# Kernel tuning notes

Hardware: AMD Instinct MI355X
Metric: run time of the kernel (lower is better)

## Reference

```python
import jax, jax.numpy as jnp
import numpy as np

V, D, H, L, F, B, S = 512, 512, 8, 6, 2048, 8, 1024
DK = D // H
EPS = 1e-5


def _positional_encoding(max_len, d_model):
    pos = np.arange(max_len, dtype=np.float32)[:, None]
    div = np.exp(np.arange(0, d_model, 2, dtype=np.float32) * (-np.log(10000.0) / d_model))
    pe = np.zeros((max_len, d_model), dtype=np.float32)
    pe[:, 0::2] = np.sin(pos * div)
    pe[:, 1::2] = np.cos(pos * div)
    return jnp.asarray(pe)


def setup_inputs() -> dict:
    key = jax.random.key(0)
    ks = jax.random.split(key, 24)
    xavier = lambda k, shp: jax.random.normal(k, shp, jnp.float32) * np.sqrt(2.0 / (shp[-2] + shp[-1]))
    inp = {
        "input_ids": jax.random.randint(ks[0], (B, S), 0, V),
        "emb": jax.random.normal(ks[1], (V, D), jnp.float32) * 0.02,
        "pe": _positional_encoding(1024, D),
        "Wq": xavier(ks[2], (L, D, D)), "bq": jnp.zeros((L, D)),
        "Wk": xavier(ks[3], (L, D, D)), "bk": jnp.zeros((L, D)),
        "Wv": xavier(ks[4], (L, D, D)), "bv": jnp.zeros((L, D)),
        "Wo": xavier(ks[5], (L, D, D)), "bo": jnp.zeros((L, D)),
        "ln1_g": jnp.ones((L, D)), "ln1_b": jnp.zeros((L, D)),
        "W1": xavier(ks[6], (L, D, F)), "b1": jnp.zeros((L, F)),
        "W2": xavier(ks[7], (L, F, D)), "b2": jnp.zeros((L, D)),
        "ln2_g": jnp.ones((L, D)), "ln2_b": jnp.zeros((L, D)),
        "Wout": xavier(ks[8], (D, V)), "bout": jnp.zeros((V,)),
    }
    return inp


def _ln(x, g, b):
    mu = jnp.mean(x, -1, keepdims=True)
    var = jnp.mean(jnp.square(x - mu), -1, keepdims=True)
    return (x - mu) * jax.lax.rsqrt(var + EPS) * g + b


def reference(input_ids, emb, pe, Wq, bq, Wk, bk, Wv, bv, Wo, bo,
              ln1_g, ln1_b, W1, b1, W2, b2, ln2_g, ln2_b, Wout, bout):
    h = emb[input_ids] * np.sqrt(D) + pe[:S]  # [B,S,D]
    # Faithful to the original mask bug: masked_fill(mask==0, -1e9) fills the
    # LOWER triangle (incl diagonal); raw scores are kept strictly where j > i.
    r = jnp.arange(S)
    keep = r[None, :] > r[:, None]  # [S,S]

    def block(h, p):
        (wq, bq_, wk, bk_, wv, bv_, wo, bo_,
         g1, be1, w1, b1_, w2, b2_, g2, be2) = p
        split = lambda t: t.reshape(B, S, H, DK).transpose(0, 2, 1, 3)
        q = split(h @ wq + bq_)
        k = split(h @ wk + bk_)
        v = split(h @ wv + bv_)
        scores = jnp.einsum('bhqd,bhkd->bhqk', q, k) / np.sqrt(DK)
        scores = jnp.where(keep, scores, -1e9)
        a = jax.nn.softmax(scores, axis=-1)
        o = jnp.einsum('bhqk,bhkd->bhqd', a, v).transpose(0, 2, 1, 3).reshape(B, S, D)
        h = _ln(h + (o @ wo + bo_), g1, be1)
        f = jax.nn.relu(h @ w1 + b1_) @ w2 + b2_
        h = _ln(h + f, g2, be2)
        return h, None

    params = (Wq, bq, Wk, bk, Wv, bv, Wo, bo, ln1_g, ln1_b, W1, b1, W2, b2, ln2_g, ln2_b)
    h, _ = jax.lax.scan(block, h, params)
    return h @ Wout + bout  # logits [B,S,V]
```

## Files before the change

### kernel.cpp

```cpp
#include <hip/hip_runtime.h>

typedef unsigned short u16;
typedef __attribute__((ext_vector_type(8))) short bf16x8;
typedef __attribute__((ext_vector_type(4))) float f32x4;
typedef __attribute__((ext_vector_type(4))) unsigned int uint4v;
typedef __attribute__((ext_vector_type(4))) unsigned short us4;

#define NLAYER 6
#define D_MODEL 512
#define NHEAD 8
#define DKH 64
#define SEQ 1024
#define BATCH 8
#define FFN 2048
#define MROWS (BATCH * SEQ)
#define QKV_LD 1536
#define SCALE_LOG2E 0.18033688011112042f

__device__ __forceinline__ float b2f(u16 u) {
  union { unsigned u32; float f; } x; x.u32 = ((unsigned)u) << 16; return x.f;
}
__device__ __forceinline__ u16 f2b(float f) {
  union { float f; unsigned u; } x; x.f = f;
  unsigned r = x.u + 0x7FFFu + ((x.u >> 16) & 1u);
  return (u16)(r >> 16);
}
__device__ __forceinline__ void gld16(const u16* g, u16* l) {
  __builtin_amdgcn_global_load_lds(
      (const __attribute__((address_space(1))) unsigned int*)g,
      (__attribute__((address_space(3))) unsigned int*)l, 16, 0, 0);
}
__device__ __forceinline__ void barrier_raw() {
  asm volatile("" ::: "memory");
  __builtin_amdgcn_s_barrier();
  asm volatile("" ::: "memory");
}

__global__ __launch_bounds__(256) void transpose_cvt_kernel(
    const float* __restrict__ src, u16* __restrict__ dst, int K, int N, size_t dstZ,
    float scale)
{
  __shared__ float t[32][33];
  const int z = blockIdx.z;
  src += (size_t)z * K * N;
  dst += (size_t)z * dstZ;
  const int n0 = blockIdx.x * 32, k0 = blockIdx.y * 32;
  const int tx = threadIdx.x, ty = threadIdx.y;
#pragma unroll
  for (int i = 0; i < 32; i += 8)
    t[ty + i][tx] = src[(size_t)(k0 + ty + i) * N + n0 + tx];
  __syncthreads();
#pragma unroll
  for (int i = 0; i < 32; i += 8)
    dst[(size_t)(n0 + ty + i) * K + k0 + tx] = f2b(t[tx][ty + i] * scale);
}

__global__ __launch_bounds__(256) void concat_bias_kernel(
    const float* __restrict__ bq, const float* __restrict__ bk,
    const float* __restrict__ bv, float* __restrict__ dst)
{
  const int l = blockIdx.x, t = threadIdx.x;
#pragma unroll
  for (int j = t; j < 512; j += 256) {
    dst[l * QKV_LD + j]        = bq[l * 512 + j] * SCALE_LOG2E;
    dst[l * QKV_LD + 512 + j]  = bk[l * 512 + j];
    dst[l * QKV_LD + 1024 + j] = bv[l * 512 + j];
  }
}

__global__ __launch_bounds__(256) void embed_kernel(
    const int* __restrict__ ids, const float* __restrict__ emb,
    const float* __restrict__ pe, float* __restrict__ Hf, u16* __restrict__ Hb)
{
  const int row = blockIdx.x;
  const int s = row & (SEQ - 1);
  const int id = ids[row];
  const int tid = threadIdx.x;
#pragma unroll
  for (int u = 0; u < 2; ++u) {
    const int d = tid + u * 256;
    float v = emb[(size_t)id * D_MODEL + d] * 22.62741699796952f + pe[(size_t)s * D_MODEL + d];
    Hf[(size_t)row * D_MODEL + d] = v;
    Hb[(size_t)row * D_MODEL + d] = f2b(v);
  }
}

template<int BMT, bool RELU, bool OUTF, bool OUTB, bool VT>
__global__ __launch_bounds__(256) void gemm_kernel(
    const u16* __restrict__ A, const u16* __restrict__ Bt,
    const float* __restrict__ bias,
    float* __restrict__ Cf, u16* __restrict__ Cb, u16* __restrict__ Vtp,
    int M, int N, int K)
{
  constexpr int IT = BMT / 32;
  constexpr int AHALF = BMT * 64;
  constexpr int BHALF = 128 * 64;
  __shared__ __align__(16) u16 As[2 * AHALF];
  __shared__ __align__(16) u16 Bs[2 * BHALF];
  const int tid = threadIdx.x;
  const int bm = blockIdx.x * BMT, bn = blockIdx.y * 128;
  const int wave = tid >> 6, lane = tid & 63;
  const int lm = lane & 15, quad = lane >> 4;
  const int wm = (wave & 1) * (BMT / 2), wn = (wave >> 1) * 64;

  const int sr = tid >> 3;
  const int sc = (tid & 7) ^ (sr & 7);
  const u16* Ap = A  + (size_t)(bm + sr) * K + sc * 8;
  const u16* Bp = Bt + (size_t)(bn + sr) * K + sc * 8;
  u16* lA = As + wave * 512;
  u16* lB = Bs + wave * 512;

  f32x4 acc[IT][4] = {};

  const int nt = K >> 6;
  auto stage = [&](int buf, int t) {
    const size_t ko = (size_t)t << 6;
#pragma unroll
    for (int p = 0; p < BMT / 32; ++p)
      gld16(Ap + (size_t)(p * 32) * K + ko, lA + buf * AHALF + p * 2048);
#pragma unroll
    for (int p = 0; p < 4; ++p)
      gld16(Bp + (size_t)(p * 32) * K + ko, lB + buf * BHALF + p * 2048);
  };

  stage(0, 0);
  __syncthreads();

  for (int t = 0; t < nt; ++t) {
    const int cur = t & 1;
    if (t + 1 < nt) stage(cur ^ 1, t + 1);
    const u16* as = As + cur * AHALF;
    const u16* bs = Bs + cur * BHALF;
#pragma unroll
    for (int kh = 0; kh < 2; ++kh) {
      bf16x8 af[IT], bg[4];
#pragma unroll
      for (int i = 0; i < IT; ++i) {
        const int row = wm + i * 16 + lm;
        af[i] = *(const bf16x8*)&as[row * 64 + (((kh * 4 + quad) ^ (row & 7)) << 3)];
      }
#pragma unroll
      for (int j = 0; j < 4; ++j) {
        const int row = wn + j * 16 + lm;
        bg[j] = *(const bf16x8*)&bs[row * 64 + (((kh * 4 + quad) ^ (row & 7)) << 3)];
      }
#pragma unroll
      for (int i = 0; i < IT; ++i)
#pragma unroll
        for (int j = 0; j < 4; ++j)
          acc[i][j] = __builtin_amdgcn_mfma_f32_16x16x32_bf16(af[i], bg[j], acc[i][j], 0, 0, 0);
    }
    __syncthreads();
  }

  const int mbase = bm + wm + quad * 4;
  const int nbase = bn + wn + lm;
#pragma unroll
  for (int i = 0; i < IT; ++i) {
#pragma unroll
    for (int j = 0; j < 4; ++j) {
      const int n = nbase + j * 16;
      const float bv = bias[n];
      float vv[4];
#pragma unroll
      for (int r = 0; r < 4; ++r) {
        float v = acc[i][j][r] + bv;
        if (RELU) v = fmaxf(v, 0.f);
        vv[r] = v;
      }
      if (VT && n >= 1024) {
        const int hh = (n - 1024) >> 6, d = (n - 1024) & 63;
        const int mm = mbase + i * 16;
        const int bb = mm >> 10, ss = mm & 1023;
        us4 pk;
#pragma unroll
        for (int r = 0; r < 4; ++r) pk[r] = f2b(vv[r]);
        *(us4*)&Vtp[(((size_t)(bb * NHEAD + hh)) * 64 + d) * SEQ + ss] = pk;
      } else {
#pragma unroll
        for (int r = 0; r < 4; ++r) {
          const int m = mbase + i * 16 + r;
          if (OUTF) Cf[(size_t)m * N + n] = vv[r];
          if (OUTB) Cb[(size_t)m * N + n] = f2b(vv[r]);
        }
      }
    }
  }
}

template<bool RELU, bool VT>
__global__ __launch_bounds__(512, 2) void gemm256_kernel(
    const u16* __restrict__ A, const u16* __restrict__ Bt,
    const float* __restrict__ bias,
    u16* __restrict__ Cb, u16* __restrict__ Vtp,
    int M, int N, int K)
{
  extern __shared__ __align__(16) u16 smem[];
  u16* Asm = smem;
  u16* Bsm = smem + 32768;
  const int tid = threadIdx.x;
  const int wave = tid >> 6, lane = tid & 63;
  const int lm = lane & 15, quad = lane >> 4, l7 = lm & 7;
  const int wm = wave >> 2, wn = wave & 3;
  const int bm = blockIdx.x * 256, bn = blockIdx.y * 256;

  const int srow = tid >> 3;
  const int scg = (tid & 7) ^ (srow & 7);
  const u16* Ap = A  + (size_t)(bm + srow) * K + scg * 8;
  const u16* Bp = Bt + (size_t)(bn + srow) * K + scg * 8;
  u16* uA = Asm + wave * 512;
  u16* uB = Bsm + wave * 512;

  f32x4 acc[8][4] = {};

  const int NT = K >> 6;
  auto stage = [&](int buf, int t) {
    const size_t ko = (size_t)t << 6;
#pragma unroll
    for (int p = 0; p < 4; ++p)
      gld16(Ap + (size_t)(p * 64) * K + ko, uA + buf * 16384 + p * 4096);
#pragma unroll
    for (int p = 0; p < 4; ++p)
      gld16(Bp + (size_t)(p * 64) * K + ko, uB + buf * 16384 + p * 4096);
  };

  stage(0, 0);
  __syncthreads();

  const int sl0 = (quad ^ l7) << 3;
  const int sl1 = ((quad + 4) ^ l7) << 3;

#pragma unroll 1
  for (int t = 0; t < NT; ++t) {
    const int cur = t & 1;
    if (t + 1 < NT) stage(cur ^ 1, t + 1);
    const u16* as_ = Asm + cur * 16384 + (wm * 128 + lm) * 64;
    const u16* bs_ = Bsm + cur * 16384 + (wn * 64 + lm) * 64;
    bf16x8 af[4][2], b01[2][2], b23[2][2];
#pragma unroll
    for (int i = 0; i < 4; ++i) {
      af[i][0] = *(const bf16x8*)&as_[i * 1024 + sl0];
      af[i][1] = *(const bf16x8*)&as_[i * 1024 + sl1];
    }
#pragma unroll
    for (int j = 0; j < 2; ++j) {
      b01[j][0] = *(const bf16x8*)&bs_[j * 1024 + sl0];
      b01[j][1] = *(const bf16x8*)&bs_[j * 1024 + sl1];
    }
    __builtin_amdgcn_s_setprio(1);
#pragma unroll
    for (int i = 0; i < 4; ++i)
#pragma unroll
      for (int j = 0; j < 2; ++j) {
        acc[i][j] = __builtin_amdgcn_mfma_f32_16x16x32_bf16(af[i][0], b01[j][0], acc[i][j], 0, 0, 0);
        acc[i][j] = __builtin_amdgcn_mfma_f32_16x16x32_bf16(af[i][1], b01[j][1], acc[i][j], 0, 0, 0);
      }
    __builtin_amdgcn_s_setprio(0);
    barrier_raw();
#pragma unroll
    for (int j = 0; j < 2; ++j) {
      b23[j][0] = *(const bf16x8*)&bs_[(j + 2) * 1024 + sl0];
      b23[j][1] = *(const bf16x8*)&bs_[(j + 2) * 1024 + sl1];
    }
    __builtin_amdgcn_s_setprio(1);
#pragma unroll
    for (int i = 0; i < 4; ++i)
#pragma unroll
      for (int j = 0; j < 2; ++j) {
        acc[i][j + 2] = __builtin_amdgcn_mfma_f32_16x16x32_bf16(af[i][0], b23[j][0], acc[i][j + 2], 0, 0, 0);
        acc[i][j + 2] = __builtin_amdgcn_mfma_f32_16x16x32_bf16(af[i][1], b23[j][1], acc[i][j + 2], 0, 0, 0);
      }
    __builtin_amdgcn_s_setprio(0);
    barrier_raw();
#pragma unroll
    for (int i = 0; i < 4; ++i) {
      af[i][0] = *(const bf16x8*)&as_[(i + 4) * 1024 + sl0];
      af[i][1] = *(const bf16x8*)&as_[(i + 4) * 1024 + sl1];
    }
    __builtin_amdgcn_s_setprio(1);
#pragma unroll
    for (int i = 0; i < 4; ++i)
#pragma unroll
      for (int j = 0; j < 2; ++j) {
        acc[i + 4][j + 2] = __builtin_amdgcn_mfma_f32_16x16x32_bf16(af[i][0], b23[j][0], acc[i + 4][j + 2], 0, 0, 0);
        acc[i + 4][j + 2] = __builtin_amdgcn_mfma_f32_16x16x32_bf16(af[i][1], b23[j][1], acc[i + 4][j + 2], 0, 0, 0);
      }
    __builtin_amdgcn_s_setprio(0);
    barrier_raw();
#pragma unroll
    for (int j = 0; j < 2; ++j) {
      b01[j][0] = *(const bf16x8*)&bs_[j * 1024 + sl0];
      b01[j][1] = *(const bf16x8*)&bs_[j * 1024 + sl1];
    }
    __builtin_amdgcn_s_setprio(1);
#pragma unroll
    for (int i = 0; i < 4; ++i)
#pragma unroll
      for (int j = 0; j < 2; ++j) {
        acc[i + 4][j] = __builtin_amdgcn_mfma_f32_16x16x32_bf16(af[i][0], b01[j][0], acc[i + 4][j], 0, 0, 0);
        acc[i + 4][j] = __builtin_amdgcn_mfma_f32_16x16x32_bf16(af[i][1], b01[j][1], acc[i + 4][j], 0, 0, 0);
      }
    __builtin_amdgcn_s_setprio(0);
    if (t + 1 < NT) {
      asm volatile("s_waitcnt vmcnt(0)" ::: "memory");
      barrier_raw();
    }
  }

  const int mbase = bm + wm * 128 + quad * 4;
  const int nbase = bn + wn * 64 + lm;
#pragma unroll
  for (int i = 0; i < 8; ++i) {
#pragma unroll
    for (int j = 0; j < 4; ++j) {
      const int n = nbase + j * 16;
      const float bv = bias[n];
      float vv[4];
#pragma unroll
      for (int r = 0; r < 4; ++r) {
        float v = acc[i][j][r] + bv;
        if (RELU) v = fmaxf(v, 0.f);
        vv[r] = v;
      }
      if (VT && n >= 1024) {
        const int hh = (n - 1024) >> 6, d = (n - 1024) & 63;
        const int mm = mbase + i * 16;
        const int bb = mm >> 10, ss = mm & 1023;
        us4 pk;
#pragma unroll
        for (int r = 0; r < 4; ++r) pk[r] = f2b(vv[r]);
        *(us4*)&Vtp[(((size_t)(bb * NHEAD + hh)) * 64 + d) * SEQ + ss] = pk;
      } else {
#pragma unroll
        for (int r = 0; r < 4; ++r) {
          const int m = mbase + i * 16 + r;
          Cb[(size_t)m * N + n] = f2b(vv[r]);
        }
      }
    }
  }
}

__global__ __launch_bounds__(256) void attn_mfma_kernel(
    const u16* __restrict__ QKV, const u16* __restrict__ Vt, u16* __restrict__ O)
{
  __shared__ __align__(16) u16 Ks[64 * 64];
  __shared__ __align__(16) u16 Vs[64 * 64];
  __shared__ __align__(16) u16 Ps[4 * 16 * 64];
  const int tid = threadIdx.x;
  const int wave = tid >> 6, lane = tid & 63;
  const int quad = lane >> 4, l15 = lane & 15;
  const int l7 = l15 & 7;
  const int id = blockIdx.x;
  const int bh = id & 63;
  const int b = bh >> 3, h = bh & 7;
  const int g = id >> 6;
  const int u = g * 4 + wave;
  u16* psw = Ps + wave * (16 * 64);
  const size_t qoff = (size_t)b * SEQ * QKV_LD + h * 64;
  const size_t vtb  = (size_t)bh * 64 * SEQ;

  const int sr = tid >> 3, sc = tid & 7;
  const u16* kg0 = QKV + qoff + 512 + (size_t)sr * QKV_LD + sc * 8;
  const u16* kg1 = kg0 + (size_t)32 * QKV_LD;
  const u16* vg0 = Vt + vtb + (size_t)sr * SEQ + sc * 8;
  const u16* vg1 = vg0 + (size_t)32 * SEQ;
  const int sw = (sc ^ (sr & 7)) << 3;
  u16* ks0 = &Ks[sr * 64 + sw];
  u16* ks1 = &Ks[(sr + 32) * 64 + sw];
  u16* vs0 = &Vs[sr * 64 + sw];
  u16* vs1 = &Vs[(sr + 32) * 64 + sw];

  const u16* qp = QKV + qoff + (size_t)(u * 16 + l15) * QKV_LD + quad * 8;
  const bf16x8 qf0 = *(const bf16x8*)(qp);
  const bf16x8 qf1 = *(const bf16x8*)(qp + 32);

  f32x4 oacc[4] = {};
  float lsum[4] = {0.f, 0.f, 0.f, 0.f};

  uint4v kr0 = *(const uint4v*)(kg0 + (size_t)(g * 64) * QKV_LD);
  uint4v kr1 = *(const uint4v*)(kg1 + (size_t)(g * 64) * QKV_LD);
  uint4v vr0 = *(const uint4v*)(vg0 + g * 64);
  uint4v vr1 = *(const uint4v*)(vg1 + g * 64);

#pragma unroll 1
  for (int jt = g; jt < 16; ++jt) {
    __syncthreads();
    *(uint4v*)ks0 = kr0; *(uint4v*)ks1 = kr1;
    *(uint4v*)vs0 = vr0; *(uint4v*)vs1 = vr1;
    __syncthreads();
    if (jt < 15) {
      kr0 = *(const uint4v*)(kg0 + (size_t)((jt + 1) * 64) * QKV_LD);
      kr1 = *(const uint4v*)(kg1 + (size_t)((jt + 1) * 64) * QKV_LD);
      vr0 = *(const uint4v*)(vg0 + (jt + 1) * 64);
      vr1 = *(const uint4v*)(vg1 + (jt + 1) * 64);
    }
    f32x4 sacc[4] = {};
#pragma unroll
    for (int nt = 0; nt < 4; ++nt) {
      const int key = nt * 16 + l15, k7 = key & 7;
      bf16x8 kb0 = *(const bf16x8*)&Ks[key * 64 + ((quad ^ k7) << 3)];
      bf16x8 kb1 = *(const bf16x8*)&Ks[key * 64 + (((quad + 4) ^ k7) << 3)];
      sacc[nt] = __builtin_amdgcn_mfma_f32_16x16x32_bf16(qf0, kb0, sacc[nt], 0, 0, 0);
      sacc[nt] = __builtin_amdgcn_mfma_f32_16x16x32_bf16(qf1, kb1, sacc[nt], 0, 0, 0);
    }
    const bool diag = (jt == g);
#pragma unroll
    for (int nt = 0; nt < 4; ++nt)
#pragma unroll
      for (int r = 0; r < 4; ++r) {
        float pv = __builtin_amdgcn_exp2f(sacc[nt][r]);
        if (diag) {
          const int i = u * 16 + quad * 4 + r;
          const int j = jt * 64 + nt * 16 + l15;
          pv = (j > i) ? pv : 0.f;
        }
        lsum[r] += pv;
        const int qr = quad * 4 + r;
        const int j2 = nt * 16 + l15;
        psw[qr * 64 + (((j2 >> 3) ^ (qr & 7)) << 3) + (j2 & 7)] = f2b(pv);
      }
    bf16x8 pf0 = *(const bf16x8*)&psw[l15 * 64 + (((quad + 0) ^ l7) << 3)];
    bf16x8 pf1 = *(const bf16x8*)&psw[l15 * 64 + (((quad + 4) ^ l7) << 3)];
#pragma unroll
    for (int nt = 0; nt < 4; ++nt) {
      const int d = nt * 16 + l15, d7 = d & 7;
      bf16x8 vb0 = *(const bf16x8*)&Vs[d * 64 + ((quad ^ d7) << 3)];
      bf16x8 vb1 = *(const bf16x8*)&Vs[d * 64 + (((quad + 4) ^ d7) << 3)];
      oacc[nt] = __builtin_amdgcn_mfma_f32_16x16x32_bf16(pf0, vb0, oacc[nt], 0, 0, 0);
      oacc[nt] = __builtin_amdgcn_mfma_f32_16x16x32_bf16(pf1, vb1, oacc[nt], 0, 0, 0);
    }
  }

#pragma unroll
  for (int o = 1; o < 16; o <<= 1)
#pragma unroll
    for (int r = 0; r < 4; ++r) lsum[r] += __shfl_xor(lsum[r], o, 16);
  float rl[4];
#pragma unroll
  for (int r = 0; r < 4; ++r) rl[r] = 1.0f / lsum[r];
#pragma unroll
  for (int nt = 0; nt < 4; ++nt)
#pragma unroll
    for (int r = 0; r < 4; ++r) {
      const int row = u * 16 + quad * 4 + r;
      O[(size_t)(b * SEQ + row) * D_MODEL + h * DKH + nt * 16 + l15] = f2b(oacc[nt][r] * rl[r]);
    }
}

__global__ __launch_bounds__(256) void vmean_kernel(
    const u16* __restrict__ Vt, u16* __restrict__ O)
{
  const int bh = blockIdx.x, tid = threadIdx.x;
  const int d = tid >> 2, sc = (tid & 3) * 256;
  const u16* p = Vt + ((size_t)bh * 64 + d) * SEQ + sc;
  float s = 0.f;
#pragma unroll 8
  for (int i = 0; i < 256; ++i) s += b2f(p[i]);
  s += __shfl_xor(s, 1, 64);
  s += __shfl_xor(s, 2, 64);
  if ((tid & 3) == 0) {
    const int b = bh >> 3, h = bh & 7;
    O[((size_t)b * SEQ + SEQ - 1) * D_MODEL + h * 64 + d] = f2b(s * (1.f / SEQ));
  }
}

__global__ __launch_bounds__(256) void add_ln_kernel(
    const float* __restrict__ Hin, const u16* __restrict__ T,
    const float* __restrict__ g, const float* __restrict__ bta,
    float* __restrict__ Hout, u16* __restrict__ Hb)
{
  __shared__ float red[8];
  const int row = blockIdx.x, tid = threadIdx.x;
  const int wave = tid >> 6, lane = tid & 63;
  const size_t base = (size_t)row * D_MODEL;
  const float x0 = Hin[base + tid] + b2f(T[base + tid]);
  const float x1 = Hin[base + tid + 256] + b2f(T[base + tid + 256]);
  float s = x0 + x1;
#pragma unroll
  for (int o = 32; o > 0; o >>= 1) s += __shfl_xor(s, o, 64);
  if (lane == 0) red[wave] = s;
  __syncthreads();
  const float mu = (red[0] + red[1] + red[2] + red[3]) * (1.f / 512.f);
  const float d0 = x0 - mu, d1 = x1 - mu;
  float v = d0 * d0 + d1 * d1;
#pragma unroll
  for (int o = 32; o > 0; o >>= 1) v += __shfl_xor(v, o, 64);
  if (lane == 0) red[4 + wave] = v;
  __syncthreads();
  const float var = (red[4] + red[5] + red[6] + red[7]) * (1.f / 512.f);
  const float rs = rsqrtf(var + 1e-5f);
  const float y0 = d0 * rs * g[tid] + bta[tid];
  const float y1 = d1 * rs * g[tid + 256] + bta[tid + 256];
  Hout[base + tid] = y0;
  Hout[base + tid + 256] = y1;
  Hb[base + tid] = f2b(y0);
  Hb[base + tid + 256] = f2b(y1);
}

extern "C" void kernel_launch(void* const* d_in, const int* in_sizes, int n_in,
                              void* d_out, int out_size, void* d_ws, size_t ws_size,
                              hipStream_t stream) {
  (void)in_sizes; (void)n_in; (void)out_size; (void)ws_size;
  const int*   ids  = (const int*)  d_in[0];
  const float* emb  = (const float*)d_in[1];
  const float* pe   = (const float*)d_in[2];
  const float* Wq   = (const float*)d_in[3];
  const float* bq   = (const float*)d_in[4];
  const float* Wk   = (const float*)d_in[5];
  const float* bk   = (const float*)d_in[6];
  const float* Wv   = (const float*)d_in[7];
  const float* bv   = (const float*)d_in[8];
  const float* Wo   = (const float*)d_in[9];
  const float* bo   = (const float*)d_in[10];
  const float* g1   = (const float*)d_in[11];
  const float* be1  = (const float*)d_in[12];
  const float* W1   = (const float*)d_in[13];
  const float* b1   = (const float*)d_in[14];
  const float* W2   = (const float*)d_in[15];
  const float* b2   = (const float*)d_in[16];
  const float* g2   = (const float*)d_in[17];
  const float* be2  = (const float*)d_in[18];
  const float* Wout = (const float*)d_in[19];
  const float* bout = (const float*)d_in[20];
  float* out = (float*)d_out;

  static int attr_set = 0;
  if (!attr_set) {
    hipFuncSetAttribute(reinterpret_cast<const void*>(&gemm256_kernel<false, true>),
                        hipFuncAttributeMaxDynamicSharedMemorySize, 131072);
    hipFuncSetAttribute(reinterpret_cast<const void*>(&gemm256_kernel<true, false>),
                        hipFuncAttributeMaxDynamicSharedMemorySize, 131072);
    attr_set = 1;
  }

  char* wsp = (char*)d_ws;
  auto alloc = [&](size_t bytes) -> char* {
    char* p = wsp; wsp += (bytes + 255) & ~(size_t)255; return p;
  };
  const size_t dd  = (size_t)D_MODEL * D_MODEL;
  const size_t df  = (size_t)D_MODEL * FFN;
  const size_t dq  = (size_t)QKV_LD * D_MODEL;
  u16* wqkv_t = (u16*)alloc(NLAYER * dq * 2);
  u16* wo_t   = (u16*)alloc(NLAYER * dd * 2);
  u16* w1_t   = (u16*)alloc(NLAYER * df * 2);
  u16* w2_t   = (u16*)alloc(NLAYER * df * 2);
  u16* wout_t = (u16*)alloc(dd * 2);
  float* bqkv = (float*)alloc(NLAYER * QKV_LD * 4);
  float* hf   = (float*)alloc((size_t)MROWS * D_MODEL * 4);
  u16*   hb   = (u16*)  alloc((size_t)MROWS * D_MODEL * 2);
  u16*   qkvb = (u16*)  alloc((size_t)MROWS * QKV_LD * 2);
  u16*   ob   = (u16*)  alloc((size_t)MROWS * D_MODEL * 2);
  u16*   vt   = (u16*)  alloc((size_t)BATCH * NHEAD * DKH * SEQ * 2);
  u16*   tb   = (u16*)  alloc((size_t)MROWS * D_MODEL * 2);
  u16*   mid  = qkvb;

  dim3 tb8(32, 8);
  transpose_cvt_kernel<<<dim3(16, 16, NLAYER), tb8, 0, stream>>>(Wq, wqkv_t,            512, 512,  dq, SCALE_LOG2E);
  transpose_cvt_kernel<<<dim3(16, 16, NLAYER), tb8, 0, stream>>>(Wk, wqkv_t + 512*512,  512, 512,  dq, 1.f);
  transpose_cvt_kernel<<<dim3(16, 16, NLAYER), tb8, 0, stream>>>(Wv, wqkv_t + 1024*512, 512, 512,  dq, 1.f);
  transpose_cvt_kernel<<<dim3(16, 16, NLAYER), tb8, 0, stream>>>(Wo, wo_t,   512, 512,  dd, 1.f);
  transpose_cvt_kernel<<<dim3(64, 16, NLAYER), tb8, 0, stream>>>(W1, w1_t,   512, 2048, df, 1.f);
  transpose_cvt_kernel<<<dim3(16, 64, NLAYER), tb8, 0, stream>>>(W2, w2_t,   2048, 512, df, 1.f);
  transpose_cvt_kernel<<<dim3(16, 16, 1),      tb8, 0, stream>>>(Wout, wout_t, 512, 512, dd, 1.f);
  concat_bias_kernel<<<NLAYER, 256, 0, stream>>>(bq, bk, bv, bqkv);

  embed_kernel<<<MROWS, 256, 0, stream>>>(ids, emb, pe, hf, hb);

  for (int l = 0; l < NLAYER; ++l) {
    gemm256_kernel<false, true><<<dim3(32, 6), 512, 131072, stream>>>(
        hb, wqkv_t + l * dq, bqkv + l * QKV_LD, qkvb, vt, MROWS, QKV_LD, 512);
    attn_mfma_kernel<<<1024, 256, 0, stream>>>(qkvb, vt, ob);
    vmean_kernel<<<64, 256, 0, stream>>>(vt, ob);
    gemm_kernel<64, false, false, true, false><<<dim3(128, 4), 256, 0, stream>>>(
        ob, wo_t + l * dd, bo + l * 512, nullptr, tb, nullptr, MROWS, 512, 512);
    add_ln_kernel<<<MROWS, 256, 0, stream>>>(hf, tb, g1 + l * 512, be1 + l * 512, hf, hb);
    gemm256_kernel<true, false><<<dim3(32, 8), 512, 131072, stream>>>(
        hb, w1_t + l * df, b1 + l * 2048, mid, nullptr, MROWS, 2048, 512);
    gemm_kernel<64, false, false, true, false><<<dim3(128, 4), 256, 0, stream>>>(
        mid, w2_t + l * df, b2 + l * 512, nullptr, tb, nullptr, MROWS, 512, 2048);
    add_ln_kernel<<<MROWS, 256, 0, stream>>>(hf, tb, g2 + l * 512, be2 + l * 512, hf, hb);
  }
  gemm_kernel<64, false, true, false, false><<<dim3(128, 4), 256, 0, stream>>>(
      hb, wout_t, bout, out, nullptr, nullptr, MROWS, 512, 512);
}
```

Before: 1.026 ms.

## Fuse output-projection and FFN2 GEMMs with residual add and LayerNorm

Replaces the N=512 GEMMs plus separate add_ln kernels with a full-row GEMM kernel (32 rows x 512 cols per block) that adds bias and residual and computes LayerNorm in its epilogue, writing fp32 and bf16 hidden state directly. This removes the intermediate bf16 tensor round trip and two launches per layer. The V-mean fix-up for the last row is also folded into the attention kernel, dropping another launch. In exchange it launches only 256 blocks with a large 138KB LDS footprint, and the whole weight panel is reloaded per small row tile, which may reduce parallelism and reuse. Variance is computed as E[x^2]-mu^2.

```diff
diff --git a/kernel.cpp b/kernel.cpp
--- a/kernel.cpp
+++ b/kernel.cpp
@@ -82,109 +82,6 @@
     float v = emb[(size_t)id * D_MODEL + d] * 22.62741699796952f + pe[(size_t)s * D_MODEL + d];
     Hf[(size_t)row * D_MODEL + d] = v;
     Hb[(size_t)row * D_MODEL + d] = f2b(v);
-  }
-}
-
-template<int BMT, bool RELU, bool OUTF, bool OUTB, bool VT>
-__global__ __launch_bounds__(256) void gemm_kernel(
-    const u16* __restrict__ A, const u16* __restrict__ Bt,
-    const float* __restrict__ bias,
-    float* __restrict__ Cf, u16* __restrict__ Cb, u16* __restrict__ Vtp,
-    int M, int N, int K)
-{
-  constexpr int IT = BMT / 32;
-  constexpr int AHALF = BMT * 64;
-  constexpr int BHALF = 128 * 64;
-  __shared__ __align__(16) u16 As[2 * AHALF];
-  __shared__ __align__(16) u16 Bs[2 * BHALF];
-  const int tid = threadIdx.x;
-  const int bm = blockIdx.x * BMT, bn = blockIdx.y * 128;
-  const int wave = tid >> 6, lane = tid & 63;
-  const int lm = lane & 15, quad = lane >> 4;
-  const int wm = (wave & 1) * (BMT / 2), wn = (wave >> 1) * 64;
-
-  const int sr = tid >> 3;
-  const int sc = (tid & 7) ^ (sr & 7);
-  const u16* Ap = A  + (size_t)(bm + sr) * K + sc * 8;
-  const u16* Bp = Bt + (size_t)(bn + sr) * K + sc * 8;
-  u16* lA = As + wave * 512;
-  u16* lB = Bs + wave * 512;
-
-  f32x4 acc[IT][4] = {};
-
-  const int nt = K >> 6;
-  auto stage = [&](int buf, int t) {
-    const size_t ko = (size_t)t << 6;
-#pragma unroll
-    for (int p = 0; p < BMT / 32; ++p)
-      gld16(Ap + (size_t)(p * 32) * K + ko, lA + buf * AHALF + p * 2048);
-#pragma unroll
-    for (int p = 0; p < 4; ++p)
-      gld16(Bp + (size_t)(p * 32) * K + ko, lB + buf * BHALF + p * 2048);
-  };
-
-  stage(0, 0);
-  __syncthreads();
-
-  for (int t = 0; t < nt; ++t) {
-    const int cur = t & 1;
-    if (t + 1 < nt) stage(cur ^ 1, t + 1);
-    const u16* as = As + cur * AHALF;
-    const u16* bs = Bs + cur * BHALF;
-#pragma unroll
-    for (int kh = 0; kh < 2; ++kh) {
-      bf16x8 af[IT], bg[4];
-#pragma unroll
-      for (int i = 0; i < IT; ++i) {
-        const int row = wm + i * 16 + lm;
-        af[i] = *(const bf16x8*)&as[row * 64 + (((kh * 4 + quad) ^ (row & 7)) << 3)];
-      }
-#pragma unroll
-      for (int j = 0; j < 4; ++j) {
-        const int row = wn + j * 16 + lm;
-        bg[j] = *(const bf16x8*)&bs[row * 64 + (((kh * 4 + quad) ^ (row & 7)) << 3)];
-      }
-#pragma unroll
-      for (int i = 0; i < IT; ++i)
-#pragma unroll
-        for (int j = 0; j < 4; ++j)
-          acc[i][j] = __builtin_amdgcn_mfma_f32_16x16x32_bf16(af[i], bg[j], acc[i][j], 0, 0, 0);
-    }
-    __syncthreads();
-  }
-
-  const int mbase = bm + wm + quad * 4;
-  const int nbase = bn + wn + lm;
-#pragma unroll
-  for (int i = 0; i < IT; ++i) {
-#pragma unroll
-    for (int j = 0; j < 4; ++j) {
-      const int n = nbase + j * 16;
-      const float bv = bias[n];
-      float vv[4];
-#pragma unroll
-      for (int r = 0; r < 4; ++r) {
-        float v = acc[i][j][r] + bv;
-        if (RELU) v = fmaxf(v, 0.f);
-        vv[r] = v;
-      }
-      if (VT && n >= 1024) {
-        const int hh = (n - 1024) >> 6, d = (n - 1024) & 63;
-        const int mm = mbase + i * 16;
-        const int bb = mm >> 10, ss = mm & 1023;
-        us4 pk;
-#pragma unroll
-        for (int r = 0; r < 4; ++r) pk[r] = f2b(vv[r]);
-        *(us4*)&Vtp[(((size_t)(bb * NHEAD + hh)) * 64 + d) * SEQ + ss] = pk;
-      } else {
-#pragma unroll
-        for (int r = 0; r < 4; ++r) {
-          const int m = mbase + i * 16 + r;
-          if (OUTF) Cf[(size_t)m * N + n] = vv[r];
-          if (OUTB) Cb[(size_t)m * N + n] = f2b(vv[r]);
-        }
-      }
-    }
   }
 }
 
@@ -338,6 +235,149 @@
         }
       }
     }
+  }
+}
+
+template<bool LN>
+__global__ __launch_bounds__(512, 2) void gemm_ln_kernel(
+    const u16* __restrict__ A, const u16* __restrict__ Bt,
+    const float* __restrict__ bias,
+    const float* __restrict__ gw, const float* __restrict__ bw,
+    float* __restrict__ Hf, u16* __restrict__ Hb, float* __restrict__ Cf,
+    int K)
+{
+  extern __shared__ __align__(16) u16 smem[];
+  u16* Asm = smem;
+  u16* Bsm = smem + 4096;
+  float* red = (float*)(smem + 69632);
+  const int tid = threadIdx.x;
+  const int wave = tid >> 6, lane = tid & 63;
+  const int lm = lane & 15, quad = lane >> 4, l7 = lm & 7;
+  const int bm = blockIdx.x * 32;
+
+  const int srow = tid >> 3;
+  const int scg = (tid & 7) ^ (srow & 7);
+  const u16* Ap = A  + (size_t)(bm + srow) * K + scg * 8;
+  const u16* Bp = Bt + (size_t)srow * K + scg * 8;
+  u16* uA = Asm + wave * 512;
+  u16* uB = Bsm + wave * 512;
+
+  f32x4 acc[2][4] = {};
+  const int NT = K >> 6;
+  auto stage = [&](int buf, int t) {
+    const size_t ko = (size_t)t << 6;
+    if (wave < 4) gld16(Ap + ko, uA + buf * 2048);
+#pragma unroll
+    for (int p = 0; p < 8; ++p)
+      gld16(Bp + (size_t)(p * 64) * K + ko, uB + buf * 32768 + p * 4096);
+  };
+
+  stage(0, 0);
+  __syncthreads();
+
+#pragma unroll 1
+  for (int t = 0; t < NT; ++t) {
+    const int cur = t & 1;
+    if (t + 1 < NT) stage(cur ^ 1, t + 1);
+    const u16* as_ = Asm + cur * 2048 + lm * 64;
+    const u16* bs_ = Bsm + cur * 32768 + (wave * 64 + lm) * 64;
+#pragma unroll
+    for (int kh = 0; kh < 2; ++kh) {
+      const int slot = ((kh * 4 + quad) ^ l7) << 3;
+      bf16x8 af[2], bg[4];
+      af[0] = *(const bf16x8*)&as_[slot];
+      af[1] = *(const bf16x8*)&as_[1024 + slot];
+#pragma unroll
+      for (int j = 0; j < 4; ++j)
+        bg[j] = *(const bf16x8*)&bs_[j * 1024 + slot];
+#pragma unroll
+      for (int i = 0; i < 2; ++i)
+#pragma unroll
+        for (int j = 0; j < 4; ++j)
+          acc[i][j] = __builtin_amdgcn_mfma_f32_16x16x32_bf16(af[i], bg[j], acc[i][j], 0, 0, 0);
+    }
+    __syncthreads();
+  }
+
+  const int col0 = wave * 64 + lm;
+  float bi[4];
+#pragma unroll
+  for (int j = 0; j < 4; ++j) bi[j] = bias[col0 + j * 16];
+
+  if (LN) {
+    float gv[4], bv[4];
+#pragma unroll
+    for (int j = 0; j < 4; ++j) { gv[j] = gw[col0 + j * 16]; bv[j] = bw[col0 + j * 16]; }
+    float x[2][4][4];
+    float ps[8], pq[8];
+#pragma unroll
+    for (int k = 0; k < 8; ++k) { ps[k] = 0.f; pq[k] = 0.f; }
+#pragma unroll
+    for (int i = 0; i < 2; ++i)
+#pragma unroll
+      for (int r = 0; r < 4; ++r) {
+        const int rowl = i * 16 + quad * 4 + r;
+        const size_t rb = (size_t)(bm + rowl) * D_MODEL;
+#pragma unroll
+        for (int j = 0; j < 4; ++j) {
+          float xv = acc[i][j][r] + bi[j] + Hf[rb + col0 + j * 16];
+          x[i][j][r] = xv;
+          ps[i * 4 + r] += xv;
+          pq[i * 4 + r] += xv * xv;
+        }
+      }
+#pragma unroll
+    for (int o = 1; o < 16; o <<= 1)
+#pragma unroll
+      for (int k = 0; k < 8; ++k) {
+        ps[k] += __shfl_xor(ps[k], o, 16);
+        pq[k] += __shfl_xor(pq[k], o, 16);
+      }
+    if (lm == 0) {
+#pragma unroll
+      for (int k = 0; k < 8; ++k) {
+        const int rowl = (k >> 2) * 16 + quad * 4 + (k & 3);
+        red[wave * 32 + rowl] = ps[k];
+        red[256 + wave * 32 + rowl] = pq[k];
+      }
+    }
+    __syncthreads();
+    if (tid < 32) {
+      float s = 0.f, q = 0.f;
+#pragma unroll
+      for (int w = 0; w < 8; ++w) { s += red[w * 32 + tid]; q += red[256 + w * 32 + tid]; }
+      const float mu = s * (1.f / 512.f);
+      const float var = q * (1.f / 512.f) - mu * mu;
+      red[512 + tid] = mu;
+      red[544 + tid] = rsqrtf(var + 1e-5f);
+    }
+    __syncthreads();
+#pragma unroll
+    for (int i = 0; i < 2; ++i)
+#pragma unroll
+      for (int r = 0; r < 4; ++r) {
+        const int rowl = i * 16 + quad * 4 + r;
+        const float mu = red[512 + rowl];
+        const float rs = red[544 + rowl];
+        const size_t rb = (size_t)(bm + rowl) * D_MODEL;
+#pragma unroll
+        for (int j = 0; j < 4; ++j) {
+          const float y = (x[i][j][r] - mu) * rs * gv[j] + bv[j];
+          Hf[rb + col0 + j * 16] = y;
+          Hb[rb + col0 + j * 16] = f2b(y);
+        }
+      }
+  } else {
+#pragma unroll
+    for (int i = 0; i < 2; ++i)
+#pragma unroll
+      for (int r = 0; r < 4; ++r) {
+        const int rowl = i * 16 + quad * 4 + r;
+        const size_t rb = (size_t)(bm + rowl) * D_MODEL;
+#pragma unroll
+        for (int j = 0; j < 4; ++j)
+          Cf[rb + col0 + j * 16] = acc[i][j][r] + bi[j];
+      }
   }
 }
 
@@ -446,56 +486,19 @@
       const int row = u * 16 + quad * 4 + r;
       O[(size_t)(b * SEQ + row) * D_MODEL + h * DKH + nt * 16 + l15] = f2b(oacc[nt][r] * rl[r]);
     }
-}
-
-__global__ __launch_bounds__(256) void vmean_kernel(
-    const u16* __restrict__ Vt, u16* __restrict__ O)
-{
-  const int bh = blockIdx.x, tid = threadIdx.x;
-  const int d = tid >> 2, sc = (tid & 3) * 256;
-  const u16* p = Vt + ((size_t)bh * 64 + d) * SEQ + sc;
-  float s = 0.f;
+
+  if (g == 15) {
+    __syncthreads();
+    const int d = tid >> 2, scv = (tid & 3) * 256;
+    const u16* pv = Vt + vtb + (size_t)d * SEQ + scv;
+    float s = 0.f;
 #pragma unroll 8
-  for (int i = 0; i < 256; ++i) s += b2f(p[i]);
-  s += __shfl_xor(s, 1, 64);
-  s += __shfl_xor(s, 2, 64);
-  if ((tid & 3) == 0) {
-    const int b = bh >> 3, h = bh & 7;
-    O[((size_t)b * SEQ + SEQ - 1) * D_MODEL + h * 64 + d] = f2b(s * (1.f / SEQ));
-  }
-}
-
-__global__ __launch_bounds__(256) void add_ln_kernel(
-    const float* __restrict__ Hin, const u16* __restrict__ T,
-    const float* __restrict__ g, const float* __restrict__ bta,
-    float* __restrict__ Hout, u16* __restrict__ Hb)
-{
-  __shared__ float red[8];
-  const int row = blockIdx.x, tid = threadIdx.x;
-  const int wave = tid >> 6, lane = tid & 63;
-  const size_t base = (size_t)row * D_MODEL;
-  const float x0 = Hin[base + tid] + b2f(T[base + tid]);
-  const float x1 = Hin[base + tid + 256] + b2f(T[base + tid + 256]);
-  float s = x0 + x1;
-#pragma unroll
-  for (int o = 32; o > 0; o >>= 1) s += __shfl_xor(s, o, 64);
-  if (lane == 0) red[wave] = s;
-  __syncthreads();
-  const float mu = (red[0] + red[1] + red[2] + red[3]) * (1.f / 512.f);
-  const float d0 = x0 - mu, d1 = x1 - mu;
-  float v = d0 * d0 + d1 * d1;
-#pragma unroll
-  for (int o = 32; o > 0; o >>= 1) v += __shfl_xor(v, o, 64);
-  if (lane == 0) red[4 + wave] = v;
-  __syncthreads();
-  const float var = (red[4] + red[5] + red[6] + red[7]) * (1.f / 512.f);
-  const float rs = rsqrtf(var + 1e-5f);
-  const float y0 = d0 * rs * g[tid] + bta[tid];
-  const float y1 = d1 * rs * g[tid + 256] + bta[tid + 256];
-  Hout[base + tid] = y0;
-  Hout[base + tid + 256] = y1;
-  Hb[base + tid] = f2b(y0);
-  Hb[base + tid + 256] = f2b(y1);
+    for (int i2 = 0; i2 < 256; ++i2) s += b2f(pv[i2]);
+    s += __shfl_xor(s, 1, 64);
+    s += __shfl_xor(s, 2, 64);
+    if ((tid & 3) == 0)
+      O[((size_t)b * SEQ + SEQ - 1) * D_MODEL + h * 64 + d] = f2b(s * (1.f / SEQ));
+  }
 }
 
 extern "C" void kernel_launch(void* const* d_in, const int* in_sizes, int n_in,
@@ -531,6 +534,10 @@
                         hipFuncAttributeMaxDynamicSharedMemorySize, 131072);
     hipFuncSetAttribute(reinterpret_cast<const void*>(&gemm256_kernel<true, false>),
                         hipFuncAttributeMaxDynamicSharedMemorySize, 131072);
+    hipFuncSetAttribute(reinterpret_cast<const void*>(&gemm_ln_kernel<true>),
+                        hipFuncAttributeMaxDynamicSharedMemorySize, 141568);
+    hipFuncSetAttribute(reinterpret_cast<const void*>(&gemm_ln_kernel<false>),
+                        hipFuncAttributeMaxDynamicSharedMemorySize, 141568);
     attr_set = 1;
   }
 
@@ -552,7 +559,6 @@
   u16*   qkvb = (u16*)  alloc((size_t)MROWS * QKV_LD * 2);
   u16*   ob   = (u16*)  alloc((size_t)MROWS * D_MODEL * 2);
   u16*   vt   = (u16*)  alloc((size_t)BATCH * NHEAD * DKH * SEQ * 2);
-  u16*   tb   = (u16*)  alloc((size_t)MROWS * D_MODEL * 2);
   u16*   mid  = qkvb;
 
   dim3 tb8(32, 8);
@@ -571,16 +577,15 @@
     gemm256_kernel<false, true><<<dim3(32, 6), 512, 131072, stream>>>(
         hb, wqkv_t + l * dq, bqkv + l * QKV_LD, qkvb, vt, MROWS, QKV_LD, 512);
     attn_mfma_kernel<<<1024, 256, 0, stream>>>(qkvb, vt, ob);
-    vmean_kernel<<<64, 256, 0, stream>>>(vt, ob);
-    gemm_kernel<64, false, false, true, false><<<dim3(128, 4), 256, 0, stream>>>(
-        ob, wo_t + l * dd, bo + l * 512, nullptr, tb, nullptr, MROWS, 512, 512);
-    add_ln_kernel<<<MROWS, 256, 0, stream>>>(hf, tb, g1 + l * 512, be1 + l * 512, hf, hb);
+    gemm_ln_kernel<true><<<256, 512, 141568, stream>>>(
+        ob, wo_t + l * dd, bo + l * 512, g1 + l * 512, be1 + l * 512,
+        hf, hb, nullptr, 512);
     gemm256_kernel<true, false><<<dim3(32, 8), 512, 131072, stream>>>(
         hb, w1_t + l * df, b1 + l * 2048, mid, nullptr, MROWS, 2048, 512);
-    gemm_kernel<64, false, false, true, false><<<dim3(128, 4), 256, 0, stream>>>(
-        mid, w2_t + l * df, b2 + l * 512, nullptr, tb, nullptr, MROWS, 512, 2048);
-    add_ln_kernel<<<MROWS, 256, 0, stream>>>(hf, tb, g2 + l * 512, be2 + l * 512, hf, hb);
-  }
-  gemm_kernel<64, false, true, false, false><<<dim3(128, 4), 256, 0, stream>>>(
-      hb, wout_t, bout, out, nullptr, nullptr, MROWS, 512, 512);
-}
+    gemm_ln_kernel<true><<<256, 512, 141568, stream>>>(
+        mid, w2_t + l * df, b2 + l * 512, g2 + l * 512, be2 + l * 512,
+        hf, hb, nullptr, 2048);
+  }
+  gemm_ln_kernel<false><<<256, 512, 141568, stream>>>(
+      hb, wout_t, bout, nullptr, nullptr, nullptr, nullptr, out, 512);
+}
```

Result: faster. 991.3 us (-3.4%).
